# Kernel optimization log

Hardware: AMD Instinct MI355X
Metric: run time of the kernel (lower is better)

Reference implementation:

```python
import jax, jax.numpy as jnp
import numpy as np
from jax import lax

NUM_CLASSES = 10
NUM_ITER = 3
CAP_DIM = 8       # primary capsule dim
OUT_CAP_DIM = 16  # digit capsule dim
NUM_MAP = 32      # 256 / 8
NUM_PRIM = 144    # 12*12


def squash(x, axis=-1):
    s2 = jnp.sum(x * x, axis=axis, keepdims=True)
    return (s2 / (1.0 + s2)) * x / jnp.sqrt(s2 + 1e-8)


def conv2d(x, w, b):
    y = lax.conv_general_dilated(x, w, (1, 1), 'VALID',
                                 dimension_numbers=('NCHW', 'OIHW', 'NCHW'))
    return y + b[None, :, None, None]


def setup_inputs() -> dict:
    key = jax.random.key(0)
    ks = jax.random.split(key, 13)
    B = 128
    return {
        'imgs': jax.random.uniform(ks[0], (B, 1, 28, 28), dtype=jnp.float32),
        'conv1_w': jax.random.normal(ks[1], (256, 1, 9, 9), jnp.float32) * 0.05,
        'conv1_b': jnp.zeros((256,), jnp.float32),
        'conv2_w': jax.random.normal(ks[2], (256, 256, 9, 9), jnp.float32) * 0.02,
        'conv2_b': jnp.zeros((256,), jnp.float32),
        # non-shared routing weights: [num_prim_map, num_prim_cap, num_classes, out_dim, in_dim]
        'W_digit': jax.random.normal(ks[3], (NUM_MAP, NUM_PRIM, NUM_CLASSES, OUT_CAP_DIM, CAP_DIM), jnp.float32),
        'dec_w1': jax.random.normal(ks[4], (OUT_CAP_DIM * NUM_CLASSES, 512), jnp.float32) * 0.05,
        'dec_b1': jnp.zeros((512,), jnp.float32),
        'dec_w2': jax.random.normal(ks[5], (512, 1024), jnp.float32) * 0.04,
        'dec_b2': jnp.zeros((1024,), jnp.float32),
        'dec_w3': jax.random.normal(ks[6], (1024, 784), jnp.float32) * 0.03,
        'dec_b3': jnp.zeros((784,), jnp.float32),
    }


def capsnet_fwd(imgs, conv1_w, conv1_b, conv2_w, conv2_b, W_digit,
                dec_w1, dec_b1, dec_w2, dec_b2, dec_w3, dec_b3):
    B = imgs.shape[0]
    # conv1 + relu: [B,256,20,20]
    x = jax.nn.relu(conv2d(imgs, conv1_w, conv1_b))
    # primary caps conv: [B,256,12,12]
    p = conv2d(x, conv2_w, conv2_b)
    # view [B, cap_dim, num_map, 12, 12] -> [B, num_map, 144, cap_dim]
    p = p.reshape(B, CAP_DIM, NUM_MAP, NUM_PRIM)
    p = jnp.transpose(p, (0, 2, 3, 1))
    u = squash(p, axis=-1)  # [B, 32, 144, 8]

    # u_hat[b,m,p,c,o] = W[m,p,c,o,i] * u[b,m,p,i]  (broadcast instead of repeat)
    u_hat = jnp.einsum('mpcoi,bmpi->bmpco', W_digit, u)
    u_hat = u_hat.reshape(B, NUM_MAP * NUM_PRIM, NUM_CLASSES, OUT_CAP_DIM)  # [B,4608,10,16]

    # dynamic routing
    b_ij = jnp.zeros((B, NUM_MAP * NUM_PRIM, NUM_CLASSES), u_hat.dtype)
    v = None
    for i in range(NUM_ITER):
        c_ij = jax.nn.softmax(b_ij, axis=1)                     # over input capsules
        s_j = jnp.einsum('bnc,bncd->bcd', c_ij, u_hat)          # [B,10,16]
        v = squash(s_j, axis=-1)
        if i != NUM_ITER - 1:
            b_ij = b_ij + jnp.einsum('bncd,bcd->bnc', u_hat, v)  # agreement

    # v: [B,10,16]
    v_length = jnp.sqrt(jnp.sum(v * v, axis=-1))                 # [B,10]
    y_pred = jnp.argmax(v_length, axis=1)
    y_pred_ohe = jax.nn.one_hot(y_pred, NUM_CLASSES, dtype=jnp.int32)

    masked = (v * y_pred_ohe.astype(v.dtype)[:, :, None]).reshape(B, -1)  # [B,160]
    h = jax.nn.relu(masked @ dec_w1 + dec_b1)
    h = jax.nn.relu(h @ dec_w2 + dec_b2)
    img_reconst = jax.nn.sigmoid(h @ dec_w3 + dec_b3)            # [B,784]
    return y_pred_ohe, img_reconst, v_length


def reference(imgs, conv1_w, conv1_b, conv2_w, conv2_b, W_digit,
              dec_w1, dec_b1, dec_w2, dec_b2, dec_w3, dec_b3):
    return capsnet_fwd(imgs, conv1_w, conv1_b, conv2_w, conv2_b, W_digit,
                       dec_w1, dec_b1, dec_w2, dec_b2, dec_w3, dec_b3)
```

## Files before the change

### kernel.cpp

```cpp
#include <hip/hip_runtime.h>
#include <cstdint>
#include <cstddef>

#define BB 128
#define NMAP 32
#define NPRIM 144
#define NCAP 4608
#define NCLS 10
#define ODIM 16
#define IDIM 8

#define WS_X1H  0
#define WS_X1L  6553600
#define WS_BH   13107200
#define WS_P    18415616
#define WS_U    23134208
#define WS_V    27852800
#define WS_H1   27873280
#define WS_H2   27938816
#define WS_CLS  28069888

#define OUT_REC  1280
#define OUT_LEN  101632

typedef __attribute__((ext_vector_type(8))) short short8;
typedef __attribute__((ext_vector_type(4))) float f32x4;

static __device__ __forceinline__ ushort f2bf(float f) {
    uint u = __float_as_uint(f);
    u = (u + 0x7FFFu + ((u >> 16) & 1u)) >> 16;
    return (ushort)u;
}
static __device__ __forceinline__ float bf2f(ushort h) {
    return __uint_as_float(((uint)h) << 16);
}

static __device__ __forceinline__ void gload16(const ushort* g, ushort* l) {
    __builtin_amdgcn_global_load_lds(
        (const __attribute__((address_space(1))) void*)g,
        (__attribute__((address_space(3))) void*)l, 16, 0, 0);
}


__global__ __launch_bounds__(256) void k_conv1(const float* __restrict__ img,
                                               const float* __restrict__ w,
                                               const float* __restrict__ bias,
                                               ushort* __restrict__ x1h,
                                               ushort* __restrict__ x1l) {
    __shared__ float simg[252];
    int bi = blockIdx.x;
    int y = bi % 20;
    int b = bi / 20;
    int oc = threadIdx.x;
    if (threadIdx.x < 252)
        simg[threadIdx.x] = img[(size_t)b * 784 + y * 28 + threadIdx.x];
    __syncthreads();

    float acc[20];
    float bv = bias[oc];
#pragma unroll
    for (int x = 0; x < 20; ++x) acc[x] = bv;
    const float* wp = w + oc * 81;
#pragma unroll
    for (int kh = 0; kh < 9; ++kh) {
        float r[28];
#pragma unroll
        for (int j = 0; j < 28; ++j) r[j] = simg[kh * 28 + j];
#pragma unroll
        for (int kw = 0; kw < 9; ++kw) {
            float wv = wp[kh * 9 + kw];
#pragma unroll
            for (int x = 0; x < 20; ++x)
                acc[x] = fmaf(wv, r[x + kw], acc[x]);
        }
    }
    size_t base = ((size_t)b * 400 + y * 20) * 256 + oc;
#pragma unroll
    for (int x = 0; x < 20; ++x) {
        float v = fmaxf(acc[x], 0.f);
        ushort h = f2bf(v);
        ushort lo = f2bf(v - bf2f(h));
        x1h[base + (size_t)x * 256] = h;
        x1l[base + (size_t)x * 256] = lo;
    }
}

__global__ __launch_bounds__(256) void k_prep_w2(const float* __restrict__ w2,
                                                 ushort* __restrict__ bpk) {
    int blk = blockIdx.x;
    int icc = blk >> 5, kq = (blk >> 3) & 3, ocg = blk & 7;
    int tid = threadIdx.x;
    int ocl = tid >> 3, ic8 = tid & 7;
    int oc = ocg * 32 + ocl;
    int ic = icc * 32 + kq * 8 + ic8;
    const float* src = w2 + ((size_t)oc * 256 + ic) * 81;
    size_t dbase = (size_t)icc * 16384 + (size_t)kq * 2048 + (size_t)oc * 8 + ic8;
#pragma unroll 9
    for (int t = 0; t < 81; ++t) {
        float v = src[t];
        ushort h = f2bf(v);
        ushort lo = f2bf(v - bf2f(h));
        bpk[(size_t)t * 131072 + dbase] = h;
        bpk[(size_t)t * 131072 + dbase + 8192] = lo;
    }
}

static __device__ __forceinline__ f32x4 mfma16(short8 a, short8 b, f32x4 c) {
    return __builtin_amdgcn_mfma_f32_16x16x32_bf16(a, b, c, 0, 0, 0);
}


template<int NMF>
static __device__ __forceinline__ void tap_body32(
    f32x4 (&acc)[5][4], const ushort* A_lds, const ushort* Bc,
    const int* celloff, int tapoff, const int* bro) {
    short8 ah[5], al[5], bh[4], bl[4];
#pragma unroll
    for (int i = 0; i < NMF; ++i) {
        ah[i] = *(const short8*)(A_lds + tapoff + celloff[i]);
        al[i] = *(const short8*)(A_lds + 16000 + tapoff + celloff[i]);
    }
#pragma unroll
    for (int j = 0; j < 4; ++j) {
        bh[j] = *(const short8*)(Bc + bro[j]);
        bl[j] = *(const short8*)(Bc + 4096 + bro[j]);
    }
#pragma unroll
    for (int i = 0; i < NMF; ++i)
#pragma unroll
        for (int j = 0; j < 4; ++j)
            acc[i][j] = mfma16(ah[i], bh[j], acc[i][j]);
#pragma unroll
    for (int i = 0; i < NMF; ++i)
#pragma unroll
        for (int j = 0; j < 4; ++j)
            acc[i][j] = mfma16(ah[i], bl[j], acc[i][j]);
#pragma unroll
    for (int i = 0; i < NMF; ++i)
#pragma unroll
        for (int j = 0; j < 4; ++j)
            acc[i][j] = mfma16(al[i], bh[j], acc[i][j]);
}

template<int MF0, int NMF>
static __device__ __forceinline__ void conv2s_epi4(
    const f32x4 (&acc)[5][4], const float* __restrict__ bias,
    float* __restrict__ p, int b, int oc0, int nh, int r, int kq) {
#pragma unroll
    for (int j = 0; j < 4; ++j) {
        int oc = oc0 + (nh * 4 + j) * 16 + r;
        float bv = bias[oc];
#pragma unroll
        for (int i = 0; i < NMF; ++i) {
            int row = b * 144 + (MF0 + i) * 16 + kq * 4;
#pragma unroll
            for (int reg = 0; reg < 4; ++reg)
                p[(size_t)(row + reg) * 256 + oc] = acc[i][j][reg] + bv;
        }
    }
}

__global__ __launch_bounds__(512, 2) void k_conv2s(
    const ushort* __restrict__ x1h, const ushort* __restrict__ x1l,
    const ushort* __restrict__ bpk,
    const float* __restrict__ bias, float* __restrict__ p) {
    __shared__ __align__(16) ushort A_lds[32000];
    __shared__ __align__(16) ushort Bb[32768];

    const int tid = threadIdx.x;
    const int lane = tid & 63;
    const int wv = tid >> 6;
    const int tp = wv >> 2;
    const int mh = (wv >> 1) & 1;
    const int nh = wv & 1;
    const int b  = blockIdx.x >> 1;
    const int nt = blockIdx.x & 1;
    const int oc0 = nt * 128;
    const int r = lane & 15, kq = lane >> 4;
    const int MF0r = mh ? 5 : 0;

    int celloff[5];
#pragma unroll
    for (int i = 0; i < 5; ++i) {
        int lm = (MF0r + i) * 16 + r;
        celloff[i] = ((lm / 12) * 20 + (lm % 12)) * 40 + kq * 8;
    }
    int bro[4];
#pragma unroll
    for (int j = 0; j < 4; ++j)
        bro[j] = kq * 1024 + ((nh * 4 + j) * 16 + r) * 8;

    const int comp_w = wv >> 2, kq_w = wv & 3;
    const ushort* gB0 = bpk + comp_w * 8192 + kq_w * 2048 + oc0 * 8 + lane * 8;
    ushort* lB0 = Bb + comp_w * 4096 + kq_w * 1024;

    f32x4 acc[5][4];
#pragma unroll
    for (int i = 0; i < 5; ++i)
#pragma unroll
        for (int j = 0; j < 4; ++j)
            acc[i][j] = (f32x4){0.f, 0.f, 0.f, 0.f};

    for (int icc = 0; icc < 8; ++icc) {
        const size_t gicc = (size_t)icc * 16384;
#pragma unroll
        for (int rd = 0; rd < 7; ++rd) {
            int idx = rd * 512 + tid;
            if (idx < 3200) {
                int comp = (idx >= 1600) ? 1 : 0;
                int ci = idx - comp * 1600;
                int cell = ci >> 2, cc = ci & 3;
                const ushort* src = (comp ? x1l : x1h) +
                    ((size_t)b * 400 + cell) * 256 + icc * 32 + cc * 8;
                short8 val = *(const short8*)src;
                *(short8*)(A_lds + comp * 16000 + cell * 40 + cc * 8) = val;
            }
        }
        gload16(gB0 + gicc, lB0);
        gload16(gB0 + gicc + 512, lB0 + 512);
        gload16(gB0 + gicc + 131072, lB0 + 8192);
        gload16(gB0 + gicc + 131072 + 512, lB0 + 8192 + 512);
        __syncthreads();

#pragma unroll 1
        for (int ph = 0; ph < 39; ++ph) {
            const int T = ph * 2;
            {
                size_t g2 = (size_t)(T + 2) * 131072 + gicc;
                ushort* d2 = lB0 + ((T + 2) & 3) * 8192;
                gload16(gB0 + g2, d2);
                gload16(gB0 + g2 + 512, d2 + 512);
                size_t g3 = g2 + 131072;
                ushort* d3 = lB0 + ((T + 3) & 3) * 8192;
                gload16(gB0 + g3, d3);
                gload16(gB0 + g3 + 512, d3 + 512);
            }
            const int tn = T + tp;
            const int kh = tn / 9, kw = tn - kh * 9;
            const int tapoff = (kh * 20 + kw) * 40;
            const ushort* Bc = Bb + (tn & 3) * 8192;
            if (mh == 0) tap_body32<5>(acc, A_lds, Bc, celloff, tapoff, bro);
            else         tap_body32<4>(acc, A_lds, Bc, celloff, tapoff, bro);
            __syncthreads();
        }
        {
            size_t g80 = (size_t)80 * 131072 + gicc;
            gload16(gB0 + g80, lB0);
            gload16(gB0 + g80 + 512, lB0 + 512);
            const int tn = 78 + tp;
            const int tapoff = (8 * 20 + (6 + tp)) * 40;
            const ushort* Bc = Bb + (tn & 3) * 8192;
            if (mh == 0) tap_body32<5>(acc, A_lds, Bc, celloff, tapoff, bro);
            else         tap_body32<4>(acc, A_lds, Bc, celloff, tapoff, bro);
            __syncthreads();
            if (tp == 0) {
                if (mh == 0) tap_body32<5>(acc, A_lds, Bb, celloff, (8 * 20 + 8) * 40, bro);
                else         tap_body32<4>(acc, A_lds, Bb, celloff, (8 * 20 + 8) * 40, bro);
            }
            __syncthreads();
        }
    }

    const int wvq = mh * 2 + nh;
    float* red = (wvq < 2) ? ((float*)A_lds + wvq * 5120)
                           : ((float*)Bb + (wvq - 2) * 5120);
    const int NMFr = mh ? 4 : 5;
    if (tp == 1) {
#pragma unroll
        for (int i = 0; i < 5; ++i) {
            if (i < NMFr)
#pragma unroll
                for (int j = 0; j < 4; ++j)
                    *(f32x4*)(red + ((i * 4 + j) * 64 + lane) * 4) = acc[i][j];
        }
    }
    __syncthreads();
    if (tp == 0) {
#pragma unroll
        for (int i = 0; i < 5; ++i) {
            if (i < NMFr)
#pragma unroll
                for (int j = 0; j < 4; ++j) {
                    f32x4 o = *(const f32x4*)(red + ((i * 4 + j) * 64 + lane) * 4);
                    acc[i][j] += o;
                }
        }
        if (mh == 0) conv2s_epi4<0, 5>(acc, bias, p, b, oc0, nh, r, kq);
        else         conv2s_epi4<5, 4>(acc, bias, p, b, oc0, nh, r, kq);
    }
}

__global__ __launch_bounds__(256) void k_squash(const float* __restrict__ p,
                                                float* __restrict__ u) {
    int id = blockIdx.x * 256 + threadIdx.x;
    int n = id % NCAP;
    int b = id / NCAP;
    int m = n / NPRIM, pos = n - m * NPRIM;
    const float* pp = p + ((size_t)b * 144 + pos) * 256 + m;
    float pv[8];
    float s2 = 0.f;
#pragma unroll
    for (int i = 0; i < 8; ++i) {
        pv[i] = pp[i * 32];
        s2 = fmaf(pv[i], pv[i], s2);
    }
    float f = (s2 / (1.f + s2)) / sqrtf(s2 + 1e-8f);
    float4 a = make_float4(f * pv[0], f * pv[1], f * pv[2], f * pv[3]);
    float4 c = make_float4(f * pv[4], f * pv[5], f * pv[6], f * pv[7]);
    float4* up = (float4*)(u + (size_t)id * 8);
    up[0] = a;
    up[1] = c;
}

__global__ __launch_bounds__(256) void k_prep_wt(const float* __restrict__ Wd,
                                                 float* __restrict__ Wt) {
    __shared__ float S[64][129];
    int c = blockIdx.x % NCLS;
    int nt = blockIdx.x / NCLS;
    int n0 = nt * 64;
    int tid = threadIdx.x;
#pragma unroll
    for (int rep = 0; rep < 32; ++rep) {
        int idx = rep * 256 + tid;
        int nl = idx >> 7, oi = idx & 127;
        S[nl][oi] = Wd[(size_t)(n0 + nl) * 1280 + c * 128 + oi];
    }
    __syncthreads();
#pragma unroll
    for (int rep = 0; rep < 32; ++rep) {
        int idx = rep * 256 + tid;
        int oi = idx >> 6, nl = idx & 63;
        Wt[((size_t)c * 128 + oi) * NCAP + n0 + nl] = S[nl][oi];
    }
}

__global__ __launch_bounds__(256) void k_route5(const float* __restrict__ u,
                                                const float* __restrict__ Wt,
                                                float* __restrict__ v_out) {
    __shared__ float part[4][2][17];
    __shared__ float sums[2][17];
    __shared__ float vsh[2][16];
    int c = blockIdx.x % NCLS;
    int bg = blockIdx.x / NCLS;
    int b0 = bg * 2;
    int tid = threadIdx.x;
    int lane = tid & 63, wvi = tid >> 6;
    const float* WtC = Wt + (size_t)c * 128 * NCAP;

    float bij[18][2];
#pragma unroll
    for (int j = 0; j < 18; ++j) { bij[j][0] = 0.f; bij[j][1] = 0.f; }

    for (int iter = 0; iter < 3; ++iter) {
        float sZ[2] = {0.f, 0.f};
        float sS[2][16];
#pragma unroll
        for (int o = 0; o < 16; ++o) { sS[0][o] = 0.f; sS[1][o] = 0.f; }

        for (int j = 0; j < 18; ++j) {
            int n = j * 256 + tid;
            const float4* up0 = (const float4*)(u + ((size_t)b0 * NCAP + n) * 8);
            const float4* up1 = (const float4*)(u + ((size_t)(b0 + 1) * NCAP + n) * 8);
            float4 a0 = up0[0], a1 = up0[1];
            float4 c0 = up1[0], c1 = up1[1];
            float u0[8] = {a0.x, a0.y, a0.z, a0.w, a1.x, a1.y, a1.z, a1.w};
            float u1[8] = {c0.x, c0.y, c0.z, c0.w, c1.x, c1.y, c1.z, c1.w};
            float uh[2][16];
#pragma unroll
            for (int o = 0; o < 16; ++o) {
                float s0 = 0.f, s1 = 0.f;
#pragma unroll
                for (int i = 0; i < 8; ++i) {
                    float w = WtC[(size_t)(o * 8 + i) * NCAP + n];
                    s0 = fmaf(w, u0[i], s0);
                    s1 = fmaf(w, u1[i], s1);
                }
                uh[0][o] = s0;
                uh[1][o] = s1;
            }
#pragma unroll
            for (int bb = 0; bb < 2; ++bb) {
                float e;
                if (iter == 0) {
                    e = 1.f;
                } else {
                    float agr = 0.f;
#pragma unroll
                    for (int o = 0; o < 16; ++o) agr = fmaf(uh[bb][o], vsh[bb][o], agr);
                    bij[j][bb] += agr;
                    e = __expf(bij[j][bb]);
                }
                sZ[bb] += e;
#pragma unroll
                for (int o = 0; o < 16; ++o) sS[bb][o] = fmaf(e, uh[bb][o], sS[bb][o]);
            }
        }

#pragma unroll
        for (int bb = 0; bb < 2; ++bb) {
            float z = sZ[bb];
#pragma unroll
            for (int d = 32; d >= 1; d >>= 1) z += __shfl_xor(z, d, 64);
            if (lane == 0) part[wvi][bb][0] = z;
#pragma unroll
            for (int o = 0; o < 16; ++o) {
                float s = sS[bb][o];
#pragma unroll
                for (int d = 32; d >= 1; d >>= 1) s += __shfl_xor(s, d, 64);
                if (lane == 0) part[wvi][bb][1 + o] = s;
            }
        }
        __syncthreads();
        if (tid < 34) {
            int bb = tid / 17, k = tid % 17;
            float s = 0.f;
#pragma unroll
            for (int w4 = 0; w4 < 4; ++w4) s += part[w4][bb][k];
            sums[bb][k] = s;
        }
        __syncthreads();
        if (tid < 2) {
            float Z = sums[tid][0];
            float s[16];
            float s2 = 0.f;
#pragma unroll
            for (int o = 0; o < 16; ++o) {
                s[o] = sums[tid][1 + o] / Z;
                s2 = fmaf(s[o], s[o], s2);
            }
            float f = (s2 / (1.f + s2)) / sqrtf(s2 + 1e-8f);
#pragma unroll
            for (int o = 0; o < 16; ++o) vsh[tid][o] = f * s[o];
        }
        __syncthreads();
    }
    if (tid < 32) {
        int bb = tid >> 4, o = tid & 15;
        v_out[((size_t)(b0 + bb) * NCLS + c) * 16 + o] = vsh[bb][o];
    }
}

__global__ __launch_bounds__(64) void k_head(const float* __restrict__ v,
                                             float* __restrict__ out,
                                             int* __restrict__ cls_ws) {
    __shared__ float len2[NCLS];
    __shared__ int cls_sh;
    int b = blockIdx.x, tid = threadIdx.x;
    if (tid < NCLS) {
        float s2 = 0.f;
#pragma unroll
        for (int o = 0; o < 16; ++o) {
            float t = v[((size_t)b * NCLS + tid) * 16 + o];
            s2 = fmaf(t, t, s2);
        }
        len2[tid] = s2;
        out[OUT_LEN + b * NCLS + tid] = sqrtf(s2);
    }
    __syncthreads();
    if (tid == 0) {
        int best = 0;
        float bv = len2[0];
        for (int c2 = 1; c2 < NCLS; ++c2)
            if (len2[c2] > bv) { bv = len2[c2]; best = c2; }
        cls_sh = best;
        cls_ws[b] = best;
    }
    __syncthreads();
    if (tid < NCLS) out[b * NCLS + tid] = (tid == cls_sh) ? 1.0f : 0.0f;
}

__global__ __launch_bounds__(256) void k_dec1(const float* __restrict__ v,
                                              const int* __restrict__ cls_ws,
                                              const float* __restrict__ w1,
                                              const float* __restrict__ b1,
                                              float* __restrict__ h1) {
    int id = blockIdx.x * 256 + threadIdx.x;
    int j = id % 512, b = id / 512;
    int cls = cls_ws[b];
    const float* vp = v + ((size_t)b * NCLS + cls) * 16;
    float acc = b1[j];
#pragma unroll
    for (int o = 0; o < 16; ++o)
        acc = fmaf(vp[o], w1[(size_t)(cls * 16 + o) * 512 + j], acc);
    h1[id] = fmaxf(acc, 0.f);
}

__global__ __launch_bounds__(256) void k_dec2(const float* __restrict__ h1,
                                              const float* __restrict__ w2,
                                              const float* __restrict__ b2,
                                              float* __restrict__ h2) {
    __shared__ float hs[512];
    int bi = blockIdx.x;
    int jc = bi % 4;
    int b = bi / 4;
    int tid = threadIdx.x;
    hs[tid] = h1[b * 512 + tid];
    hs[tid + 256] = h1[b * 512 + tid + 256];
    __syncthreads();
    int j = jc * 256 + tid;
    float acc = b2[j];
#pragma unroll 8
    for (int k = 0; k < 512; ++k)
        acc = fmaf(hs[k], w2[(size_t)k * 1024 + j], acc);
    h2[b * 1024 + j] = fmaxf(acc, 0.f);
}

__global__ __launch_bounds__(256) void k_dec3(const float* __restrict__ h2,
                                              const float* __restrict__ w3,
                                              const float* __restrict__ b3,
                                              float* __restrict__ out) {
    __shared__ float hs[1024];
    int bi = blockIdx.x;
    int jc = bi % 4;
    int b = bi / 4;
    int tid = threadIdx.x;
#pragma unroll
    for (int t = 0; t < 4; ++t) hs[tid + t * 256] = h2[b * 1024 + tid + t * 256];
    __syncthreads();
    int j = jc * 256 + tid;
    if (j < 784) {
        float acc = b3[j];
#pragma unroll 8
        for (int k = 0; k < 1024; ++k)
            acc = fmaf(hs[k], w3[(size_t)k * 784 + j], acc);
        out[OUT_REC + b * 784 + j] = 1.f / (1.f + __expf(-acc));
    }
}

extern "C" void kernel_launch(void* const* d_in, const int* in_sizes, int n_in,
                              void* d_out, int out_size, void* d_ws, size_t ws_size,
                              hipStream_t stream) {
    const float* imgs = (const float*)d_in[0];
    const float* c1w  = (const float*)d_in[1];
    const float* c1b  = (const float*)d_in[2];
    const float* c2w  = (const float*)d_in[3];
    const float* c2b  = (const float*)d_in[4];
    const float* Wd   = (const float*)d_in[5];
    const float* dw1  = (const float*)d_in[6];
    const float* db1  = (const float*)d_in[7];
    const float* dw2  = (const float*)d_in[8];
    const float* db2  = (const float*)d_in[9];
    const float* dw3  = (const float*)d_in[10];
    const float* db3  = (const float*)d_in[11];

    float* out = (float*)d_out;
    float* ws  = (float*)d_ws;
    ushort* x1h = (ushort*)(ws + WS_X1H);
    ushort* x1l = (ushort*)(ws + WS_X1L);
    ushort* bpk = (ushort*)(ws + WS_BH);
    float* p    = ws + WS_P;
    float* u    = ws + WS_U;
    float* v    = ws + WS_V;
    float* h1   = ws + WS_H1;
    float* h2   = ws + WS_H2;
    int*   cls  = (int*)(ws + WS_CLS);
    float* wt32 = ws + WS_X1H;

    k_conv1<<<BB * 20, 256, 0, stream>>>(imgs, c1w, c1b, x1h, x1l);
    k_prep_w2<<<256, 256, 0, stream>>>(c2w, bpk);
    k_conv2s<<<BB * 2, 512, 0, stream>>>(x1h, x1l, bpk, c2b, p);
    k_squash<<<BB * NCAP / 256, 256, 0, stream>>>(p, u);
    k_prep_wt<<<720, 256, 0, stream>>>(Wd, wt32);
    k_route5<<<(BB / 2) * NCLS, 256, 0, stream>>>(u, wt32, v);
    k_head<<<BB, 64, 0, stream>>>(v, out, cls);
    k_dec1<<<BB * 512 / 256, 256, 0, stream>>>(v, cls, dw1, db1, h1);
    k_dec2<<<BB * 4, 256, 0, stream>>>(h1, dw2, db2, h2);
    k_dec3<<<BB * 4, 256, 0, stream>>>(h2, dw3, db3, out);
}
```

Before: 1.184 ms.

## Software-pipeline conv2 tap loop with register double-buffered fragments and 6-slot LDS ring

Restructures the primary-caps conv main loop so LDS fragment loads for the next tap pair are issued while MFMAs for the current pair run, using two register fragment sets. The B staging ring grows from 4 to 6 slots so global prefetch runs further ahead. Launch bounds drop from 2 to 1 blocks per CU, since the larger LDS and register footprint leaves room for only one 512-thread block. The aim is to hide LDS and global latency behind matrix work, at the cost of occupancy.

```diff
diff --git a/kernel.cpp b/kernel.cpp
--- a/kernel.cpp
+++ b/kernel.cpp
@@ -110,36 +110,54 @@
 }
 
 
+struct Frag { short8 ah[5], al[5], bh[4], bl[4]; };
+
 template<int NMF>
-static __device__ __forceinline__ void tap_body32(
-    f32x4 (&acc)[5][4], const ushort* A_lds, const ushort* Bc,
-    const int* celloff, int tapoff, const int* bro) {
-    short8 ah[5], al[5], bh[4], bl[4];
+static __device__ __forceinline__ void pre_frag(
+    Frag& f, const ushort* A_lds, const ushort* Bb, int tn,
+    const int* celloff, const int* bro) {
+    int kh = tn / 9, kw = tn - kh * 9;
+    int tapoff = (kh * 20 + kw) * 40;
+    const ushort* Bc = Bb + (tn % 6) * 8192;
 #pragma unroll
     for (int i = 0; i < NMF; ++i) {
-        ah[i] = *(const short8*)(A_lds + tapoff + celloff[i]);
-        al[i] = *(const short8*)(A_lds + 16000 + tapoff + celloff[i]);
+        f.ah[i] = *(const short8*)(A_lds + tapoff + celloff[i]);
+        f.al[i] = *(const short8*)(A_lds + 16000 + tapoff + celloff[i]);
     }
 #pragma unroll
     for (int j = 0; j < 4; ++j) {
-        bh[j] = *(const short8*)(Bc + bro[j]);
-        bl[j] = *(const short8*)(Bc + 4096 + bro[j]);
-    }
+        f.bh[j] = *(const short8*)(Bc + bro[j]);
+        f.bl[j] = *(const short8*)(Bc + 4096 + bro[j]);
+    }
+}
+
+template<int NMF>
+static __device__ __forceinline__ void mfma_frag(f32x4 (&acc)[5][4], const Frag& f) {
 #pragma unroll
     for (int i = 0; i < NMF; ++i)
 #pragma unroll
         for (int j = 0; j < 4; ++j)
-            acc[i][j] = mfma16(ah[i], bh[j], acc[i][j]);
+            acc[i][j] = mfma16(f.ah[i], f.bh[j], acc[i][j]);
 #pragma unroll
     for (int i = 0; i < NMF; ++i)
 #pragma unroll
         for (int j = 0; j < 4; ++j)
-            acc[i][j] = mfma16(ah[i], bl[j], acc[i][j]);
+            acc[i][j] = mfma16(f.ah[i], f.bl[j], acc[i][j]);
 #pragma unroll
     for (int i = 0; i < NMF; ++i)
 #pragma unroll
         for (int j = 0; j < 4; ++j)
-            acc[i][j] = mfma16(al[i], bh[j], acc[i][j]);
+            acc[i][j] = mfma16(f.al[i], f.bh[j], acc[i][j]);
+}
+
+static __device__ __forceinline__ void stage_tap(
+    const ushort* gB0, ushort* lB0, int tn, size_t gicc) {
+    if (tn <= 80) {
+        size_t g = (size_t)tn * 131072 + gicc;
+        ushort* d = lB0 + (tn % 6) * 8192;
+        gload16(gB0 + g, d);
+        gload16(gB0 + g + 512, d + 512);
+    }
 }
 
 template<int MF0, int NMF>
@@ -160,12 +178,12 @@
     }
 }
 
-__global__ __launch_bounds__(512, 2) void k_conv2s(
+__global__ __launch_bounds__(512, 1) void k_conv2s(
     const ushort* __restrict__ x1h, const ushort* __restrict__ x1l,
     const ushort* __restrict__ bpk,
     const float* __restrict__ bias, float* __restrict__ p) {
     __shared__ __align__(16) ushort A_lds[32000];
-    __shared__ __align__(16) ushort Bb[32768];
+    __shared__ __align__(16) ushort Bb[49152];
 
     const int tid = threadIdx.x;
     const int lane = tid & 63;
@@ -201,6 +219,8 @@
         for (int j = 0; j < 4; ++j)
             acc[i][j] = (f32x4){0.f, 0.f, 0.f, 0.f};
 
+    Frag fX, fY;
+
     for (int icc = 0; icc < 8; ++icc) {
         const size_t gicc = (size_t)icc * 16384;
 #pragma unroll
@@ -216,51 +236,47 @@
                 *(short8*)(A_lds + comp * 16000 + cell * 40 + cc * 8) = val;
             }
         }
-        gload16(gB0 + gicc, lB0);
-        gload16(gB0 + gicc + 512, lB0 + 512);
-        gload16(gB0 + gicc + 131072, lB0 + 8192);
-        gload16(gB0 + gicc + 131072 + 512, lB0 + 8192 + 512);
+        stage_tap(gB0, lB0, 0, gicc);
+        stage_tap(gB0, lB0, 1, gicc);
+        stage_tap(gB0, lB0, 2, gicc);
+        stage_tap(gB0, lB0, 3, gicc);
         __syncthreads();
+        if (mh == 0) pre_frag<5>(fX, A_lds, Bb, tp, celloff, bro);
+        else         pre_frag<4>(fX, A_lds, Bb, tp, celloff, bro);
 
 #pragma unroll 1
-        for (int ph = 0; ph < 39; ++ph) {
-            const int T = ph * 2;
-            {
-                size_t g2 = (size_t)(T + 2) * 131072 + gicc;
-                ushort* d2 = lB0 + ((T + 2) & 3) * 8192;
-                gload16(gB0 + g2, d2);
-                gload16(gB0 + g2 + 512, d2 + 512);
-                size_t g3 = g2 + 131072;
-                ushort* d3 = lB0 + ((T + 3) & 3) * 8192;
-                gload16(gB0 + g3, d3);
-                gload16(gB0 + g3 + 512, d3 + 512);
-            }
-            const int tn = T + tp;
-            const int kh = tn / 9, kw = tn - kh * 9;
-            const int tapoff = (kh * 20 + kw) * 40;
-            const ushort* Bc = Bb + (tn & 3) * 8192;
-            if (mh == 0) tap_body32<5>(acc, A_lds, Bc, celloff, tapoff, bro);
-            else         tap_body32<4>(acc, A_lds, Bc, celloff, tapoff, bro);
+        for (int it = 0; it < 20; ++it) {
+            const int T = it * 4;
+            stage_tap(gB0, lB0, T + 4, gicc);
+            stage_tap(gB0, lB0, T + 5, gicc);
+            if (mh == 0) {
+                mfma_frag<5>(acc, fX);
+                pre_frag<5>(fY, A_lds, Bb, T + 2 + tp, celloff, bro);
+            } else {
+                mfma_frag<4>(acc, fX);
+                pre_frag<4>(fY, A_lds, Bb, T + 2 + tp, celloff, bro);
+            }
             __syncthreads();
-        }
-        {
-            size_t g80 = (size_t)80 * 131072 + gicc;
-            gload16(gB0 + g80, lB0);
-            gload16(gB0 + g80 + 512, lB0 + 512);
-            const int tn = 78 + tp;
-            const int tapoff = (8 * 20 + (6 + tp)) * 40;
-            const ushort* Bc = Bb + (tn & 3) * 8192;
-            if (mh == 0) tap_body32<5>(acc, A_lds, Bc, celloff, tapoff, bro);
-            else         tap_body32<4>(acc, A_lds, Bc, celloff, tapoff, bro);
+            stage_tap(gB0, lB0, T + 6, gicc);
+            stage_tap(gB0, lB0, T + 7, gicc);
+            const int tnX = T + 4 + tp;
+            const bool doPre = (tnX <= 80);
+            if (mh == 0) {
+                mfma_frag<5>(acc, fY);
+                if (doPre) pre_frag<5>(fX, A_lds, Bb, tnX, celloff, bro);
+            } else {
+                mfma_frag<4>(acc, fY);
+                if (doPre) pre_frag<4>(fX, A_lds, Bb, tnX, celloff, bro);
+            }
             __syncthreads();
-            if (tp == 0) {
-                if (mh == 0) tap_body32<5>(acc, A_lds, Bb, celloff, (8 * 20 + 8) * 40, bro);
-                else         tap_body32<4>(acc, A_lds, Bb, celloff, (8 * 20 + 8) * 40, bro);
-            }
-            __syncthreads();
-        }
-    }
-
+        }
+        if (tp == 0) {
+            if (mh == 0) mfma_frag<5>(acc, fX);
+            else         mfma_frag<4>(acc, fX);
+        }
+    }
+
+    __syncthreads();
     const int wvq = mh * 2 + nh;
     float* red = (wvq < 2) ? ((float*)A_lds + wvq * 5120)
                            : ((float*)Bb + (wvq - 2) * 5120);
```

Result: slower. 2.019 ms (+70.6%).
